# Kernel optimization log

Hardware: AMD Instinct MI355X
Metric: run time of the kernel (lower is better)

## Reference

```python
import jax, jax.numpy as jnp
import numpy as np
import itertools

N_PTS = 3  # xyz
N_CORNERS = 8
# All 8! = 40320 permutations of the 8 corners, as flattened one-hot
# permutation matrices [P, 64] so permutation costs become one GEMM.
_PERMS = np.array(list(itertools.permutations(range(N_CORNERS))), dtype=np.int32)  # [40320, 8]
_PERM_ONEHOT = np.eye(N_CORNERS, dtype=np.float32)[_PERMS].reshape(len(_PERMS), N_CORNERS * N_CORNERS)  # [40320, 64]
PERM_ONEHOT = jnp.asarray(_PERM_ONEHOT)


def setup_inputs() -> dict:
    key = jax.random.key(0)
    k1, k2 = jax.random.split(key)
    B = 4096
    pred_corners = jax.random.normal(k1, (B, N_CORNERS, N_PTS), dtype=jnp.float32)
    target_corners = jax.random.normal(k2, (B, N_CORNERS, N_PTS), dtype=jnp.float32)
    return {"pred_corners": pred_corners, "target_corners": target_corners}


def reference(pred_corners, target_corners):
    # Pairwise Euclidean distances between pred corner i and target corner j.
    diff = pred_corners[:, :, None, :] - target_corners[:, None, :, :]  # [B, 8, 8, 3]
    dist = jnp.sqrt(jnp.sum(diff * diff, axis=-1))                      # [B, 8, 8]
    B = dist.shape[0]
    # Cost of every permutation: costs[b, p] = sum_i dist[b, i, perm_p(i)].
    costs = dist.reshape(B, N_CORNERS * N_CORNERS) @ PERM_ONEHOT.T      # [B, 40320]
    # Earth mover distance for equal-size point sets = min-cost perfect matching.
    loss = jnp.min(costs, axis=1)                                       # [B]
    return loss
```

## Files before the change

kernel.cpp:

```cpp
#include <hip/hip_runtime.h>
#include <math.h>


#define INF 1e30f
#define WAVES_PER_BLOCK 4

__global__ __launch_bounds__(256) void emd8_wave_kernel(
    const float* __restrict__ pred,
    const float* __restrict__ targ,
    float* __restrict__ out, int B) {

    const int tid  = threadIdx.x;
    const int lane = tid & 63;
    const int b    = (int)((blockIdx.x * blockDim.x + tid) >> 6);
    if (b >= B) return;

    float v = 0.0f;
    if (lane < 48) {
        v = (lane < 24) ? pred[b * 24 + lane] : targ[b * 24 + (lane - 24)];
    }

    const int i = lane >> 3, j = lane & 7;
    const float px = __shfl(v, i * 3 + 0);
    const float py = __shfl(v, i * 3 + 1);
    const float pz = __shfl(v, i * 3 + 2);
    const float tx = __shfl(v, 24 + j * 3 + 0);
    const float ty = __shfl(v, 24 + j * 3 + 1);
    const float tz = __shfl(v, 24 + j * 3 + 2);
    const float dx = px - tx, dy = py - ty, dz = pz - tz;
    const float dist = sqrtf(dx * dx + dy * dy + dz * dz);

    float r0 = (lane == 0) ? 0.0f : INF;
    float r1 = INF, r2 = INF, r3 = INF;

    #pragma unroll
    for (int k = 1; k <= 8; ++k) {
        float d[8];
        #pragma unroll
        for (int jj = 0; jj < 8; ++jj) d[jj] = __shfl(dist, (k - 1) * 8 + jj);

        float n0 = INF, n1 = INF, n2 = INF, n3 = INF;
        #pragma unroll
        for (int jj = 0; jj < 6; ++jj) {
            const float s0 = __shfl_xor(r0, 1 << jj);
            const float s1 = __shfl_xor(r1, 1 << jj);
            const float s2 = __shfl_xor(r2, 1 << jj);
            const float s3 = __shfl_xor(r3, 1 << jj);
            n0 = fminf(n0, s0 + d[jj]);
            n1 = fminf(n1, s1 + d[jj]);
            n2 = fminf(n2, s2 + d[jj]);
            n3 = fminf(n3, s3 + d[jj]);
        }
        n0 = fminf(n0, fminf(r1 + d[6], r2 + d[7]));
        n1 = fminf(n1, fminf(r0 + d[6], r3 + d[7]));
        n2 = fminf(n2, fminf(r3 + d[6], r0 + d[7]));
        n3 = fminf(n3, fminf(r2 + d[6], r1 + d[7]));
        r0 = n0; r1 = n1; r2 = n2; r3 = n3;
    }

    if (lane == 63) out[b] = r3;
}

extern "C" void kernel_launch(void* const* d_in, const int* in_sizes, int n_in,
                              void* d_out, int out_size, void* d_ws, size_t ws_size,
                              hipStream_t stream) {
    const float* pred = (const float*)d_in[0];
    const float* targ = (const float*)d_in[1];
    float* out = (float*)d_out;
    const int B = in_sizes[0] / 24;
    const int waves = B;
    const int grid  = (waves + WAVES_PER_BLOCK - 1) / WAVES_PER_BLOCK;
    emd8_wave_kernel<<<grid, 64 * WAVES_PER_BLOCK, 0, stream>>>(pred, targ, out, B);
}
```

Before: 64.35 us.

## Compute each matching with a per-thread bitmask DP held in registers

Replaces the one-wave-per-sample shuffle DP with one thread per sample. Each thread loads its corners with float4 loads, builds the 8x8 distance matrix in registers and runs a fully unrolled 256-state subset DP to get the min-cost matching. This removes the cross-lane shuffle traffic and the per-sample wave overhead. In exchange it uses very high register pressure (f[256], d[64]) and launches only B/64 single-wave blocks, so few waves are resident to hide latency.

```diff
diff --git a/kernel.cpp b/kernel.cpp
--- a/kernel.cpp
+++ b/kernel.cpp
@@ -3,62 +3,55 @@
 
 
 #define INF 1e30f
-#define WAVES_PER_BLOCK 4
 
-__global__ __launch_bounds__(256) void emd8_wave_kernel(
+__global__ __launch_bounds__(64, 1) void emd8_lane_kernel(
     const float* __restrict__ pred,
     const float* __restrict__ targ,
     float* __restrict__ out, int B) {
 
-    const int tid  = threadIdx.x;
-    const int lane = tid & 63;
-    const int b    = (int)((blockIdx.x * blockDim.x + tid) >> 6);
+    const int b = blockIdx.x * 64 + (int)threadIdx.x;
     if (b >= B) return;
 
-    float v = 0.0f;
-    if (lane < 48) {
-        v = (lane < 24) ? pred[b * 24 + lane] : targ[b * 24 + (lane - 24)];
+    float p[24], t[24];
+    const float4* __restrict__ p4 = (const float4*)(pred + (size_t)b * 24);
+    const float4* __restrict__ t4 = (const float4*)(targ + (size_t)b * 24);
+    #pragma unroll
+    for (int q = 0; q < 6; ++q) {
+        const float4 a = p4[q];
+        p[q * 4 + 0] = a.x; p[q * 4 + 1] = a.y;
+        p[q * 4 + 2] = a.z; p[q * 4 + 3] = a.w;
+        const float4 c = t4[q];
+        t[q * 4 + 0] = c.x; t[q * 4 + 1] = c.y;
+        t[q * 4 + 2] = c.z; t[q * 4 + 3] = c.w;
     }
 
-    const int i = lane >> 3, j = lane & 7;
-    const float px = __shfl(v, i * 3 + 0);
-    const float py = __shfl(v, i * 3 + 1);
-    const float pz = __shfl(v, i * 3 + 2);
-    const float tx = __shfl(v, 24 + j * 3 + 0);
-    const float ty = __shfl(v, 24 + j * 3 + 1);
-    const float tz = __shfl(v, 24 + j * 3 + 2);
-    const float dx = px - tx, dy = py - ty, dz = pz - tz;
-    const float dist = sqrtf(dx * dx + dy * dy + dz * dz);
-
-    float r0 = (lane == 0) ? 0.0f : INF;
-    float r1 = INF, r2 = INF, r3 = INF;
-
+    float d[64];
     #pragma unroll
-    for (int k = 1; k <= 8; ++k) {
-        float d[8];
+    for (int i = 0; i < 8; ++i) {
         #pragma unroll
-        for (int jj = 0; jj < 8; ++jj) d[jj] = __shfl(dist, (k - 1) * 8 + jj);
-
-        float n0 = INF, n1 = INF, n2 = INF, n3 = INF;
-        #pragma unroll
-        for (int jj = 0; jj < 6; ++jj) {
-            const float s0 = __shfl_xor(r0, 1 << jj);
-            const float s1 = __shfl_xor(r1, 1 << jj);
-            const float s2 = __shfl_xor(r2, 1 << jj);
-            const float s3 = __shfl_xor(r3, 1 << jj);
-            n0 = fminf(n0, s0 + d[jj]);
-            n1 = fminf(n1, s1 + d[jj]);
-            n2 = fminf(n2, s2 + d[jj]);
-            n3 = fminf(n3, s3 + d[jj]);
+        for (int j = 0; j < 8; ++j) {
+            const float dx = p[i * 3 + 0] - t[j * 3 + 0];
+            const float dy = p[i * 3 + 1] - t[j * 3 + 1];
+            const float dz = p[i * 3 + 2] - t[j * 3 + 2];
+            d[i * 8 + j] = sqrtf(dx * dx + dy * dy + dz * dz);
         }
-        n0 = fminf(n0, fminf(r1 + d[6], r2 + d[7]));
-        n1 = fminf(n1, fminf(r0 + d[6], r3 + d[7]));
-        n2 = fminf(n2, fminf(r3 + d[6], r0 + d[7]));
-        n3 = fminf(n3, fminf(r2 + d[6], r1 + d[7]));
-        r0 = n0; r1 = n1; r2 = n2; r3 = n3;
     }
 
-    if (lane == 63) out[b] = r3;
+    float f[256];
+    f[0] = 0.0f;
+    #pragma unroll
+    for (int m = 1; m < 256; ++m) {
+        const int row8 = (__builtin_popcount(m) - 1) * 8;
+        float best = INF;
+        #pragma unroll
+        for (int j = 0; j < 8; ++j) {
+            if ((m >> j) & 1)
+                best = fminf(best, f[m ^ (1 << j)] + d[row8 + j]);
+        }
+        f[m] = best;
+    }
+
+    out[b] = f[255];
 }
 
 extern "C" void kernel_launch(void* const* d_in, const int* in_sizes, int n_in,
@@ -68,7 +61,6 @@
     const float* targ = (const float*)d_in[1];
     float* out = (float*)d_out;
     const int B = in_sizes[0] / 24;
-    const int waves = B;
-    const int grid  = (waves + WAVES_PER_BLOCK - 1) / WAVES_PER_BLOCK;
-    emd8_wave_kernel<<<grid, 64 * WAVES_PER_BLOCK, 0, stream>>>(pred, targ, out, B);
+    const int grid = (B + 63) / 64;
+    emd8_lane_kernel<<<grid, 64, 0, stream>>>(pred, targ, out, B);
 }
```

Measured after the change: 208.3 us. +223.6%, slower.
